# Kernel tuning notes

Hardware: AMD Instinct MI355X
Metric: run time of the kernel (lower is better)

The kernel has to match this reference:

```python
import jax, jax.numpy as jnp
import numpy as np

# ---- static config ----
SCALES = [1, 2, 3, 4, 6, 9, 13, 19, 27, 40, 60, 88, 128]
L = sum(SCALES)            # 400
FIRST_L = SCALES[0]        # 1
C = 1024                   # emb_dim (C == D)
DEPTH = 8
H = 16
DH = C // H
CVAE = 64
V = 4096
ND = 256                   # node_embed_size
MLP = 4 * C
B = 32
EPS = 1e-6

_LVL = np.concatenate([np.full(pn, i, dtype=np.int32) for i, pn in enumerate(SCALES)])  # [L]
_BIAS = np.where(_LVL[:, None] >= _LVL[None, :], 0.0, -np.inf).astype(np.float32)        # [L,L]


def _ln(x):
    # LayerNorm without affine params (VAR's ln_wo_grad), eps=1e-6
    m = jnp.mean(x, axis=-1, keepdims=True)
    v = jnp.mean(jnp.square(x - m), axis=-1, keepdims=True)
    return (x - m) * jax.lax.rsqrt(v + EPS)


def setup_inputs() -> dict:
    key = jax.random.key(0)
    ks = iter(jax.random.split(key, 40))
    def p(shape, s=0.02):
        return jax.random.normal(next(ks), shape, dtype=jnp.float32) * s
    inp = {
        "x_BLCv_wo_first_l": jax.random.normal(next(ks), (B, L - FIRST_L, CVAE), jnp.float32),
        "poc_context": jax.random.normal(next(ks), (B, L, CVAE), jnp.float32),
        "poc_cond": jax.random.normal(next(ks), (B, ND), jnp.float32),
        # embedders / positional
        "word_w": p((CVAE, C)), "word_b": p((C,)),
        "poc_w": p((ND, C)), "poc_b": p((C,)),
        "pos_start": p((1, FIRST_L, C)),
        "pos_1LC": p((1, L, C)),
        "lvl_tab": p((len(SCALES), C)),
        # shared AdaLN (SiLU -> Linear(D, 6C))
        "ada_w": p((C, 6 * C)), "ada_b": p((6 * C,)),
        # per-block params, stacked over depth
        "ada_gss": p((DEPTH, 1, 1, 6, C)),
        "q_w": p((DEPTH, C, C)), "q_b": p((DEPTH, C)),
        "kv_w": p((DEPTH, C, 2 * C)), "kv_b": p((DEPTH, 2 * C)),
        "proj_w": p((DEPTH, C, C)), "proj_b": p((DEPTH, C)),
        "fc1_w": p((DEPTH, C, MLP)), "fc1_b": p((DEPTH, MLP)),
        "fc2_w": p((DEPTH, MLP, C)), "fc2_b": p((DEPTH, C)),
        # AdaLNBeforeHead (SiLU -> Linear(D, 2C)) + head
        "head_ada_w": p((C, 2 * C)), "head_ada_b": p((2 * C,)),
        "head_w": p((C, V)), "head_b": p((V,)),
    }
    return inp


def reference(x_BLCv_wo_first_l, poc_context, poc_cond,
              word_w, word_b, poc_w, poc_b, pos_start, pos_1LC, lvl_tab,
              ada_w, ada_b, ada_gss, q_w, q_b, kv_w, kv_b, proj_w, proj_b,
              fc1_w, fc1_b, fc2_w, fc2_b, head_ada_w, head_ada_b, head_w, head_b):
    lvl_idx = jnp.asarray(_LVL)
    bias = jnp.asarray(_BIAS)                      # [L,L] block scale-causal
    scale = 1.0 / np.sqrt(DH)

    cond = poc_cond @ poc_w + poc_b                # [B,C] (cond_BD == sos source)
    sos = cond[:, None, :] + pos_start             # [B,first_l,C]
    x = jnp.concatenate([sos, x_BLCv_wo_first_l @ word_w + word_b], axis=1)  # [B,L,C]
    lvl = lvl_tab[lvl_idx] + pos_1LC[0]            # [L,C]
    x = x + lvl
    poc = (poc_context @ word_w + word_b) + lvl    # [B,L,C]

    gss = jax.nn.silu(cond) @ ada_w + ada_b        # [B,6C]
    gss = gss.reshape(B, 1, 6, C)

    def block(x, params):
        ag, qw, qb, kvw, kvb, pw, pb, f1w, f1b, f2w, f2b = params
        mod = ag + gss                             # [B,1,6,C]
        g1, g2, s1, s2, sh1, sh2 = [mod[:, :, i] for i in range(6)]  # each [B,1,C]
        # cross-attention (q from modulated x, kv from poc context), scale-causal bias
        xn = _ln(x) * (1.0 + s1) + sh1
        q = (xn @ qw + qb).reshape(B, L, H, DH)
        kv = (poc @ kvw + kvb).reshape(B, L, 2, H, DH)
        k, v = kv[:, :, 0], kv[:, :, 1]
        att = jnp.einsum('bqhd,bkhd->bhqk', q, k) * scale + bias
        att = jax.nn.softmax(att, axis=-1)
        o = jnp.einsum('bhqk,bkhd->bqhd', att, v).reshape(B, L, C)
        x = x + g1 * (o @ pw + pb)
        # FFN with AdaLN modulation
        xn2 = _ln(x) * (1.0 + s2) + sh2
        hdn = jax.nn.gelu(xn2 @ f1w + f1b, approximate=False)
        x = x + g2 * (hdn @ f2w + f2b)
        return x, None

    x, _ = jax.lax.scan(block, x, (ada_gss, q_w, q_b, kv_w, kv_b, proj_w, proj_b,
                                   fc1_w, fc1_b, fc2_w, fc2_b))

    # AdaLNBeforeHead + head
    ss = jax.nn.silu(cond) @ head_ada_w + head_ada_b   # [B,2C]
    h_scale, h_shift = ss[:, None, :C], ss[:, None, C:]
    x = _ln(x) * (1.0 + h_scale) + h_shift
    logits = x @ head_w + head_b                       # [B,L,V]
    return logits
```

## Files before the change

### kernel.cpp

```cpp
#include <hip/hip_runtime.h>
#include <hip/hip_bf16.h>
#include <math.h>

#define DEV __device__ __forceinline__

typedef __attribute__((ext_vector_type(4))) float f32x4;
typedef __attribute__((ext_vector_type(8))) short bf16x8;
typedef __attribute__((ext_vector_type(4))) short s16x4;

static constexpr int Bz = 32, Lz = 400, Cz = 1024, MLPz = 4096;
static constexpr int BL = Bz * Lz;

DEV float bf2f(unsigned short u) {
  union { unsigned int i; float f; } v; v.i = ((unsigned int)u) << 16; return v.f;
}
DEV unsigned short f2bf(float f) {
  union { float f; unsigned int i; } v; v.f = f;
  unsigned int r = v.i + 0x7FFFu + ((v.i >> 16) & 1u);
  return (unsigned short)(r >> 16);
}

DEV int level_of(int l) {
  const int cum[13] = {1,3,6,10,16,25,38,57,84,124,184,272,400};
  int lv = 12;
  #pragma unroll
  for (int i = 12; i >= 0; i--) if (l < cum[i]) lv = i;
  return lv;
}
DEV int row_kmax(int l) {
  const int cum[13] = {1,3,6,10,16,25,38,57,84,124,184,272,400};
  int km = 400;
  #pragma unroll
  for (int i = 12; i >= 0; i--) if (l < cum[i]) km = cum[i];
  return km;
}

DEV void stage16(const unsigned short* g, unsigned short* l) {
#if __has_builtin(__builtin_amdgcn_global_load_lds)
  __builtin_amdgcn_global_load_lds((const __attribute__((address_space(1))) void*)g,
                                   (__attribute__((address_space(3))) void*)l, 16, 0, 0);
#else
  *(bf16x8*)l = *(const bf16x8*)g;
#endif
}

__global__ __launch_bounds__(256)
void tconv_k(const float* __restrict__ in, unsigned short* __restrict__ out, int K, int N)
{
  __shared__ float t[64][65];
  const int n0 = blockIdx.x * 64, k0 = blockIdx.y * 64;
  #pragma unroll
  for (int i = 0; i < 16; i++) {
    int idx = i * 256 + threadIdx.x;
    int r = idx >> 6, c = idx & 63;
    t[r][c] = in[(size_t)(k0 + r) * N + n0 + c];
  }
  __syncthreads();
  #pragma unroll
  for (int i = 0; i < 16; i++) {
    int idx = i * 256 + threadIdx.x;
    int rn = idx >> 6, ck = idx & 63;
    out[(size_t)(n0 + rn) * K + k0 + ck] = f2bf(t[ck][rn]);
  }
}

__global__ __launch_bounds__(256)
void tconv4_k(const float* __restrict__ qw, const float* __restrict__ kvw,
              const float* __restrict__ pjw, const float* __restrict__ f1w,
              unsigned short* __restrict__ qwt, unsigned short* __restrict__ kvwt,
              unsigned short* __restrict__ pjwt, unsigned short* __restrict__ f1wt)
{
  const int z = blockIdx.z;
  const float* in; unsigned short* out; int N;
  if (z == 0)      { in = qw;  out = qwt;  N = 1024; }
  else if (z == 1) { in = kvw; out = kvwt; N = 2048; }
  else if (z == 2) { in = pjw; out = pjwt; N = 1024; }
  else             { in = f1w; out = f1wt; N = 4096; }
  if ((int)blockIdx.x >= (N >> 6)) return;
  __shared__ float t[64][65];
  const int n0 = blockIdx.x * 64, k0 = blockIdx.y * 64;
  #pragma unroll
  for (int i = 0; i < 16; i++) {
    int idx = i * 256 + threadIdx.x;
    int r = idx >> 6, c = idx & 63;
    t[r][c] = in[(size_t)(k0 + r) * N + n0 + c];
  }
  __syncthreads();
  #pragma unroll
  for (int i = 0; i < 16; i++) {
    int idx = i * 256 + threadIdx.x;
    int rn = idx >> 6, ck = idx & 63;
    out[(size_t)(n0 + rn) * 1024 + k0 + ck] = f2bf(t[ck][rn]);
  }
}

enum { EP_BF16 = 0, EP_GELU = 1, EP_RESID = 2, EP_F32 = 3, EP_KV = 4 };

template<int MODE>
__global__ __launch_bounds__(256, 2)
void gemm2_k(const unsigned short* __restrict__ A, const unsigned short* __restrict__ Bt,
             const float* __restrict__ bias, void* __restrict__ out,
             float* __restrict__ xres, const float* __restrict__ gsh,
             const float* __restrict__ gpb, unsigned short* __restrict__ vtb,
             int N, int K)
{
  __shared__ unsigned short As[128 * 64];
  __shared__ unsigned short Bs[128 * 64];
  const int tid = threadIdx.x;
  const int lane = tid & 63, wv = tid >> 6;

  const int nwg = gridDim.x * gridDim.y;
  const int cpx = nwg >> 3;
  const int bid = blockIdx.y * gridDim.x + blockIdx.x;
  const int swz = (bid & 7) * cpx + (bid >> 3);
  const int row0 = (swz % 100) * 128, col0 = (swz / 100) * 128;

  const int wm = (wv >> 1) * 64, wn = (wv & 1) * 64;

  f32x4 acc[4][4] = {};

  for (int k0 = 0; k0 < K; k0 += 64) {
    #pragma unroll
    for (int i = 0; i < 4; i++) {
      int ch = i * 256 + tid;
      int r = ch >> 3;
      int c8 = (ch & 7) ^ (r & 7);
      stage16(A + (size_t)(row0 + r) * K + k0 + c8 * 8, As + ch * 8);
    }
    #pragma unroll
    for (int i = 0; i < 4; i++) {
      int ch = i * 256 + tid;
      int r = ch >> 3;
      int c8 = (ch & 7) ^ (r & 7);
      stage16(Bt + (size_t)(col0 + r) * K + k0 + c8 * 8, Bs + ch * 8);
    }
    __syncthreads();
    #pragma unroll
    for (int kk = 0; kk < 2; kk++) {
      bf16x8 af[4], bfr[4];
      const int bcol = kk * 64 + (lane >> 4) * 16;
      #pragma unroll
      for (int m = 0; m < 4; m++) {
        int r = wm + m * 16 + (lane & 15);
        af[m] = *(const bf16x8*)((char*)As + r * 128 + (bcol ^ ((r & 7) << 4)));
      }
      #pragma unroll
      for (int n = 0; n < 4; n++) {
        int r = wn + n * 16 + (lane & 15);
        bfr[n] = *(const bf16x8*)((char*)Bs + r * 128 + (bcol ^ ((r & 7) << 4)));
      }
      #pragma unroll
      for (int m = 0; m < 4; m++)
        #pragma unroll
        for (int n = 0; n < 4; n++)
          acc[m][n] = __builtin_amdgcn_mfma_f32_16x16x32_bf16(af[m], bfr[n], acc[m][n], 0, 0, 0);
    }
    __syncthreads();
  }

  const int rbase = row0 + wm + ((lane >> 4) << 2);
  const int cbase = col0 + wn + (lane & 15);
  #pragma unroll
  for (int n = 0; n < 4; n++) {
    int gcol = cbase + n * 16;
    float bv = bias[gcol];
    #pragma unroll
    for (int m = 0; m < 4; m++) {
      #pragma unroll
      for (int r = 0; r < 4; r++) {
        int grow = rbase + m * 16 + r;
        float v = acc[m][n][r] + bv;
        if constexpr (MODE == EP_BF16) {
          ((unsigned short*)out)[(size_t)grow * N + gcol] = f2bf(v);
        } else if constexpr (MODE == EP_GELU) {
          float g = 0.5f * v * (1.f + erff(v * 0.70710678118654752f));
          ((unsigned short*)out)[(size_t)grow * N + gcol] = f2bf(g);
        } else if constexpr (MODE == EP_RESID) {
          int b = grow / Lz;
          float g = gsh[gcol] + gpb[(size_t)b * 6144 + gcol];
          xres[(size_t)grow * Cz + gcol] += g * v;
        } else if constexpr (MODE == EP_KV) {
          if (gcol < 1024) {
            ((unsigned short*)out)[(size_t)grow * 1024 + gcol] = f2bf(v);
          } else {
            int b = grow / Lz, l = grow - b * Lz;
            int h = (gcol >> 6) & 15, d = gcol & 63;
            vtb[(((size_t)b * 16 + h) * 64 + d) * Lz + l] = f2bf(v);
          }
        } else {
          ((float*)out)[(size_t)grow * N + gcol] = v;
        }
      }
    }
  }
}

__global__ __launch_bounds__(256)
void ln_k(const float* __restrict__ x, unsigned short* __restrict__ out,
          const float* __restrict__ ssh, const float* __restrict__ spb, int sstride,
          const float* __restrict__ hsh, const float* __restrict__ hpb, int hstride)
{
  const int row = blockIdx.x, tid = threadIdx.x;
  const int b = row / Lz;
  const float* xr = x + (size_t)row * Cz;
  f32x4 v = *(const f32x4*)(xr + tid * 4);
  float s = v[0] + v[1] + v[2] + v[3];
  __shared__ float red[8];
  #pragma unroll
  for (int o = 32; o > 0; o >>= 1) s += __shfl_xor(s, o, 64);
  if ((tid & 63) == 0) red[tid >> 6] = s;
  __syncthreads();
  float mean = (red[0] + red[1] + red[2] + red[3]) * (1.f / 1024.f);
  float vs = 0.f;
  #pragma unroll
  for (int i = 0; i < 4; i++) { float d = v[i] - mean; vs += d * d; }
  #pragma unroll
  for (int o = 32; o > 0; o >>= 1) vs += __shfl_xor(vs, o, 64);
  __syncthreads();
  if ((tid & 63) == 0) red[4 + (tid >> 6)] = vs;
  __syncthreads();
  float var = (red[4] + red[5] + red[6] + red[7]) * (1.f / 1024.f);
  float rstd = rsqrtf(var + 1e-6f);
  #pragma unroll
  for (int i = 0; i < 4; i++) {
    int c = tid * 4 + i;
    float sc = (ssh ? ssh[c] : 0.f) + spb[(size_t)b * sstride + c];
    float sh = (hsh ? hsh[c] : 0.f) + hpb[(size_t)b * hstride + c];
    out[(size_t)row * Cz + c] = f2bf((v[i] - mean) * rstd * (1.f + sc) + sh);
  }
}

__global__ __launch_bounds__(512)
void attn3_k(const unsigned short* __restrict__ qb,
             const unsigned short* __restrict__ kbuf,
             const unsigned short* __restrict__ vtb,
             unsigned short* __restrict__ ob)
{
  __shared__ unsigned short Ks[400 * 64];
  __shared__ unsigned short Vt[64 * 408];
  __shared__ unsigned short Pl[8][512];
  const int bh = blockIdx.x, b = bh >> 4, h = bh & 15;
  const int qc = blockIdx.y;
  const int tid = threadIdx.x;
  const int q0 = qc * 128;
  const int nch = (row_kmax(min(q0 + 127, Lz - 1)) + 15) >> 4;

  const size_t kbase = (size_t)b * Lz * 1024 + h * 64;
  for (int i = tid; i < nch * 128; i += 512) {
    int l = i >> 3, d8 = i & 7;
    bf16x8 kr = *(const bf16x8*)&kbuf[kbase + (size_t)l * 1024 + d8 * 8];
    *(bf16x8*)((char*)Ks + l * 128 + ((d8 * 16) ^ ((l & 7) << 4))) = kr;
  }
  const size_t vbase = ((size_t)b * 16 + h) * 64 * Lz;
  for (int i = tid; i < 64 * 50; i += 512) {
    int d = i / 50, c8 = i - d * 50;
    *(bf16x8*)((char*)Vt + d * 816 + c8 * 16) = *(const bf16x8*)&vtb[vbase + (size_t)d * Lz + c8 * 8];
  }
  __syncthreads();

  const int wv = tid >> 6, lane = tid & 63, g = lane >> 4, q = lane & 15;
  const int qw0 = q0 + wv * 16;
  if (qw0 >= Lz) return;
  const int qrow = qw0 + q;
  const int my_kmax = row_kmax(qrow);
  const int nsch = (row_kmax(qw0 + 15) + 31) >> 5;

  const unsigned short* qp = qb + (size_t)(b * Lz + qrow) * Cz + h * 64;
  bf16x8 qf0 = *(const bf16x8*)(qp + g * 8);
  bf16x8 qf1 = *(const bf16x8*)(qp + 32 + g * 8);
  unsigned short* myP = &Pl[wv][0];

  float m = -1e30f, lsum = 0.f;
  f32x4 acc[4] = {};

  for (int sc = 0; sc < nsch; ++sc) {
    f32x4 st0 = {0.f,0.f,0.f,0.f}, st1 = {0.f,0.f,0.f,0.f};
    {
      int kr = sc * 32 + q;
      const char* kb = (const char*)Ks + kr * 128;
      int sw = (kr & 7) << 4;
      bf16x8 k0 = *(const bf16x8*)(kb + ((g * 16) ^ sw));
      bf16x8 k1 = *(const bf16x8*)(kb + ((64 + g * 16) ^ sw));
      st0 = __builtin_amdgcn_mfma_f32_16x16x32_bf16(k0, qf0, st0, 0, 0, 0);
      st0 = __builtin_amdgcn_mfma_f32_16x16x32_bf16(k1, qf1, st0, 0, 0, 0);
    }
    {
      int kr = sc * 32 + 16 + q;
      const char* kb = (const char*)Ks + kr * 128;
      int sw = (kr & 7) << 4;
      bf16x8 k0 = *(const bf16x8*)(kb + ((g * 16) ^ sw));
      bf16x8 k1 = *(const bf16x8*)(kb + ((64 + g * 16) ^ sw));
      st1 = __builtin_amdgcn_mfma_f32_16x16x32_bf16(k0, qf0, st1, 0, 0, 0);
      st1 = __builtin_amdgcn_mfma_f32_16x16x32_bf16(k1, qf1, st1, 0, 0, 0);
    }

    float s8[8]; float cmax = -1e30f;
    #pragma unroll
    for (int r = 0; r < 4; r++) {
      int k0g = sc * 32 + 4 * g + r;
      int k1g = k0g + 16;
      s8[r]     = (k0g < my_kmax) ? st0[r] * 0.125f : -1e30f;
      s8[4 + r] = (k1g < my_kmax) ? st1[r] * 0.125f : -1e30f;
      cmax = fmaxf(cmax, fmaxf(s8[r], s8[4 + r]));
    }
    cmax = fmaxf(cmax, __shfl_xor(cmax, 16, 64));
    cmax = fmaxf(cmax, __shfl_xor(cmax, 32, 64));
    float mnew = fmaxf(m, cmax);
    float f = __expf(m - mnew);
    float p[8], ps = 0.f;
    #pragma unroll
    for (int r = 0; r < 8; r++) { p[r] = __expf(s8[r] - mnew); ps += p[r]; }
    ps += __shfl_xor(ps, 16, 64);
    ps += __shfl_xor(ps, 32, 64);
    lsum = lsum * f + ps;
    m = mnew;
    #pragma unroll
    for (int blk = 0; blk < 4; blk++)
      #pragma unroll
      for (int j = 0; j < 4; j++) acc[blk][j] *= f;

    #pragma unroll
    for (int cp = 0; cp < 2; cp++) {
      #pragma unroll
      for (int j = 0; j < 2; j++) {
        unsigned int lo = f2bf(p[4 * cp + 2 * j]);
        unsigned int hi = f2bf(p[4 * cp + 2 * j + 1]);
        int w = 8 * cp + 2 * g + j;
        *(unsigned int*)((char*)myP + q * 64 + 4 * (w ^ q)) = lo | (hi << 16);
      }
    }

    unsigned int pw[4];
    #pragma unroll
    for (int i = 0; i < 4; i++)
      pw[i] = *(const unsigned int*)((const char*)myP + q * 64 + 4 * ((4 * g + i) ^ q));
    bf16x8 pfrag;
    #pragma unroll
    for (int i = 0; i < 4; i++) {
      pfrag[2 * i]     = (short)(pw[i] & 0xFFFF);
      pfrag[2 * i + 1] = (short)(pw[i] >> 16);
    }

    #pragma unroll
    for (int blk = 0; blk < 4; blk++) {
      bf16x8 vf = *(const bf16x8*)((const char*)Vt + (16 * blk + q) * 816 + (sc * 32 + 8 * g) * 2);
      acc[blk] = __builtin_amdgcn_mfma_f32_16x16x32_bf16(vf, pfrag, acc[blk], 0, 0, 0);
    }
  }

  float inv = 1.f / lsum;
  unsigned short* op = ob + (size_t)(b * Lz + qrow) * Cz + h * 64;
  #pragma unroll
  for (int blk = 0; blk < 4; blk++)
    #pragma unroll
    for (int r = 0; r < 4; r++)
      op[16 * blk + 4 * g + r] = f2bf(acc[blk][r] * inv);
}

__global__ __launch_bounds__(256)
void cond_k(const float* __restrict__ pc, const float* __restrict__ pw,
            const float* __restrict__ pb, float* __restrict__ cond,
            float* __restrict__ silu)
{
  const int b = blockIdx.y;
  const int n = blockIdx.x * 256 + threadIdx.x;
  __shared__ float a[256];
  a[threadIdx.x] = pc[b * 256 + threadIdx.x];
  __syncthreads();
  float s = pb[n];
  for (int k = 0; k < 256; k++) s += a[k] * pw[(size_t)k * Cz + n];
  cond[(size_t)b * Cz + n] = s;
  silu[(size_t)b * Cz + n] = s / (1.f + __expf(-s));
}

__global__ __launch_bounds__(256)
void smallmm_k(const float* __restrict__ A, const float* __restrict__ W,
               const float* __restrict__ bias, float* __restrict__ out, int N)
{
  const int b = blockIdx.y;
  const int n = blockIdx.x * 256 + threadIdx.x;
  __shared__ float a[1024];
  for (int i = threadIdx.x; i < 1024; i += 256) a[i] = A[(size_t)b * 1024 + i];
  __syncthreads();
  float s = bias[n];
  for (int k = 0; k < 1024; k++) s += a[k] * W[(size_t)k * N + n];
  out[(size_t)b * N + n] = s;
}

template<int MODE>
__global__ __launch_bounds__(256)
void embed_k(const float* __restrict__ src, const float* __restrict__ ww,
             const float* __restrict__ wb, const float* __restrict__ cond,
             const float* __restrict__ pos_start, const float* __restrict__ pos1,
             const float* __restrict__ ltab, void* __restrict__ out)
{
  const int r0 = blockIdx.x * 4;
  const int tid = threadIdx.x;
  const int b = r0 / Lz;
  __shared__ float a[4][64];
  {
    int rr = tid >> 6, k = tid & 63;
    int l = (r0 + rr) % Lz;
    float val;
    if (MODE == 0) val = (l == 0) ? 0.f : src[((size_t)b * (Lz - 1) + (l - 1)) * 64 + k];
    else           val = src[((size_t)(r0 + rr)) * 64 + k];
    a[rr][k] = val;
  }
  __syncthreads();
  #pragma unroll
  for (int ci = 0; ci < 4; ci++) {
    int c = tid + ci * 256;
    float s[4];
    #pragma unroll
    for (int rr = 0; rr < 4; rr++) {
      int l = (r0 + rr) % Lz;
      s[rr] = wb[c] + ltab[(size_t)level_of(l) * Cz + c] + pos1[(size_t)l * Cz + c];
    }
    for (int k = 0; k < 64; k++) {
      float w = ww[(size_t)k * Cz + c];
      #pragma unroll
      for (int rr = 0; rr < 4; rr++) s[rr] += a[rr][k] * w;
    }
    #pragma unroll
    for (int rr = 0; rr < 4; rr++) {
      int l = (r0 + rr) % Lz;
      if (MODE == 0) {
        float val = s[rr];
        if (l == 0) val = cond[(size_t)b * Cz + c] + pos_start[c] + ltab[c] + pos1[c];
        ((float*)out)[((size_t)(r0 + rr)) * Cz + c] = val;
      } else {
        ((unsigned short*)out)[((size_t)(r0 + rr)) * Cz + c] = f2bf(s[rr]);
      }
    }
  }
}

extern "C" void kernel_launch(void* const* d_in, const int* in_sizes, int n_in,
                              void* d_out, int out_size, void* d_ws, size_t ws_size,
                              hipStream_t stream)
{
  (void)in_sizes; (void)n_in; (void)out_size; (void)ws_size;
  const float* x_blcv   = (const float*)d_in[0];
  const float* poc_ctx  = (const float*)d_in[1];
  const float* poc_cond = (const float*)d_in[2];
  const float* word_w   = (const float*)d_in[3];
  const float* word_b   = (const float*)d_in[4];
  const float* poc_w    = (const float*)d_in[5];
  const float* poc_b    = (const float*)d_in[6];
  const float* pos_start= (const float*)d_in[7];
  const float* pos_1lc  = (const float*)d_in[8];
  const float* lvl_tab  = (const float*)d_in[9];
  const float* ada_w    = (const float*)d_in[10];
  const float* ada_b    = (const float*)d_in[11];
  const float* ada_gss  = (const float*)d_in[12];
  const float* q_w      = (const float*)d_in[13];
  const float* q_b      = (const float*)d_in[14];
  const float* kv_w     = (const float*)d_in[15];
  const float* kv_b     = (const float*)d_in[16];
  const float* proj_w   = (const float*)d_in[17];
  const float* proj_b   = (const float*)d_in[18];
  const float* fc1_w    = (const float*)d_in[19];
  const float* fc1_b    = (const float*)d_in[20];
  const float* fc2_w    = (const float*)d_in[21];
  const float* fc2_b    = (const float*)d_in[22];
  const float* head_ada_w = (const float*)d_in[23];
  const float* head_ada_b = (const float*)d_in[24];
  const float* head_w   = (const float*)d_in[25];
  const float* head_b   = (const float*)d_in[26];

  char* p = (char*)d_ws;
  auto carve = [&](size_t bytes) { void* r = (void*)p; p += (bytes + 255) & ~(size_t)255; return r; };
  float* x            = (float*)carve((size_t)BL * Cz * 4);
  unsigned short* xn  = (unsigned short*)carve((size_t)BL * Cz * 2);
  unsigned short* poc = (unsigned short*)carve((size_t)BL * Cz * 2);
  unsigned short* qbf = (unsigned short*)carve((size_t)BL * Cz * 2);
  unsigned short* kbuf= (unsigned short*)carve((size_t)BL * Cz * 2);
  unsigned short* vtb = (unsigned short*)carve((size_t)BL * Cz * 2);
  unsigned short* ob  = (unsigned short*)carve((size_t)BL * Cz * 2);
  unsigned short* hdn = (unsigned short*)carve((size_t)BL * MLPz * 2);
  unsigned short* wt  = (unsigned short*)carve((size_t)12582912 * 2);
  float* cond  = (float*)carve(32 * 1024 * 4);
  float* siluc = (float*)carve(32 * 1024 * 4);
  float* gss   = (float*)carve(32 * 6144 * 4);
  float* ss    = (float*)carve(32 * 2048 * 4);

  unsigned short* qwt  = wt;
  unsigned short* kvwt = wt + 1048576;
  unsigned short* pjwt = wt + 3145728;
  unsigned short* f1wt = wt + 4194304;
  unsigned short* f2wt = wt + 8388608;

  cond_k<<<dim3(4, 32), 256, 0, stream>>>(poc_cond, poc_w, poc_b, cond, siluc);
  smallmm_k<<<dim3(24, 32), 256, 0, stream>>>(siluc, ada_w, ada_b, gss, 6144);
  smallmm_k<<<dim3(8, 32), 256, 0, stream>>>(siluc, head_ada_w, head_ada_b, ss, 2048);
  embed_k<0><<<3200, 256, 0, stream>>>(x_blcv, word_w, word_b, cond, pos_start, pos_1lc, lvl_tab, x);
  embed_k<1><<<3200, 256, 0, stream>>>(poc_ctx, word_w, word_b, cond, pos_start, pos_1lc, lvl_tab, poc);

  for (int d = 0; d < 8; d++) {
    const float* ag = ada_gss + (size_t)d * 6144;
    tconv4_k<<<dim3(64, 16, 4), 256, 0, stream>>>(
        q_w + (size_t)d * 1048576, kv_w + (size_t)d * 2097152,
        proj_w + (size_t)d * 1048576, fc1_w + (size_t)d * 4194304,
        qwt, kvwt, pjwt, f1wt);
    tconv_k<<<dim3(16, 64), 256, 0, stream>>>(fc2_w + (size_t)d * 4194304, f2wt, 4096, 1024);

    ln_k<<<BL, 256, 0, stream>>>(x, xn, ag + 2 * 1024, gss + 2 * 1024, 6144,
                                 ag + 4 * 1024, gss + 4 * 1024, 6144);
    gemm2_k<EP_BF16><<<dim3(100, 8), 256, 0, stream>>>(
        xn, qwt, q_b + d * 1024, qbf, nullptr, nullptr, nullptr, nullptr, 1024, 1024);
    gemm2_k<EP_KV><<<dim3(100, 16), 256, 0, stream>>>(
        poc, kvwt, kv_b + d * 2048, kbuf, nullptr, nullptr, nullptr, vtb, 2048, 1024);
    attn3_k<<<dim3(512, 4), 512, 0, stream>>>(qbf, kbuf, vtb, ob);
    gemm2_k<EP_RESID><<<dim3(100, 8), 256, 0, stream>>>(
        ob, pjwt, proj_b + d * 1024, nullptr, x, ag + 0, gss + 0, nullptr, 1024, 1024);
    ln_k<<<BL, 256, 0, stream>>>(x, xn, ag + 3 * 1024, gss + 3 * 1024, 6144,
                                 ag + 5 * 1024, gss + 5 * 1024, 6144);
    gemm2_k<EP_GELU><<<dim3(100, 32), 256, 0, stream>>>(
        xn, f1wt, fc1_b + d * 4096, hdn, nullptr, nullptr, nullptr, nullptr, 4096, 1024);
    gemm2_k<EP_RESID><<<dim3(100, 8), 256, 0, stream>>>(
        hdn, f2wt, fc2_b + d * 1024, nullptr, x, ag + 1024, gss + 1024, nullptr, 1024, 4096);
  }
  ln_k<<<BL, 256, 0, stream>>>(x, xn, nullptr, ss, 2048, nullptr, ss + 1024, 2048);
  tconv_k<<<dim3(64, 16), 256, 0, stream>>>(head_w, wt, 1024, 4096);
  gemm2_k<EP_F32><<<dim3(100, 32), 256, 0, stream>>>(
      xn, wt, head_b, d_out, nullptr, nullptr, nullptr, nullptr, 4096, 1024);
}
```

Before: 6.781 ms.

## Drop GEMM tile swizzle, vectorize LN store, trim attention V staging and rescaling

The GEMM replaces its XCD-aware block swizzle with plain blockIdx row/column mapping. The LayerNorm-modulate kernel now packs four bf16 outputs into one vector store. The attention kernel stages only the V columns the query chunk needs, clamps V fragment offsets to that range, and skips the online-softmax rescale when the running max does not grow by more than a threshold. It also converts P to bf16 with a packed hardware instruction. The lazy rescale and the smaller -30000 mask constant risk numeric differences, and removing the swizzle may hurt L2 locality across chiplets.

```diff
diff --git a/kernel.cpp b/kernel.cpp
--- a/kernel.cpp
+++ b/kernel.cpp
@@ -108,13 +108,7 @@
   __shared__ unsigned short Bs[128 * 64];
   const int tid = threadIdx.x;
   const int lane = tid & 63, wv = tid >> 6;
-
-  const int nwg = gridDim.x * gridDim.y;
-  const int cpx = nwg >> 3;
-  const int bid = blockIdx.y * gridDim.x + blockIdx.x;
-  const int swz = (bid & 7) * cpx + (bid >> 3);
-  const int row0 = (swz % 100) * 128, col0 = (swz / 100) * 128;
-
+  const int row0 = blockIdx.x * 128, col0 = blockIdx.y * 128;
   const int wm = (wv >> 1) * 64, wn = (wv & 1) * 64;
 
   f32x4 acc[4][4] = {};
@@ -221,13 +215,15 @@
   __syncthreads();
   float var = (red[4] + red[5] + red[6] + red[7]) * (1.f / 1024.f);
   float rstd = rsqrtf(var + 1e-6f);
+  s16x4 o4;
   #pragma unroll
   for (int i = 0; i < 4; i++) {
     int c = tid * 4 + i;
     float sc = (ssh ? ssh[c] : 0.f) + spb[(size_t)b * sstride + c];
     float sh = (hsh ? hsh[c] : 0.f) + hpb[(size_t)b * hstride + c];
-    out[(size_t)row * Cz + c] = f2bf((v[i] - mean) * rstd * (1.f + sc) + sh);
-  }
+    o4[i] = (short)f2bf((v[i] - mean) * rstd * (1.f + sc) + sh);
+  }
+  *(s16x4*)(&out[(size_t)row * Cz + tid * 4]) = o4;
 }
 
 __global__ __launch_bounds__(512)
@@ -252,8 +248,9 @@
     *(bf16x8*)((char*)Ks + l * 128 + ((d8 * 16) ^ ((l & 7) << 4))) = kr;
   }
   const size_t vbase = ((size_t)b * 16 + h) * 64 * Lz;
-  for (int i = tid; i < 64 * 50; i += 512) {
-    int d = i / 50, c8 = i - d * 50;
+  const int vch = nch * 2;
+  for (int i = tid; i < 64 * vch; i += 512) {
+    int d = i / vch, c8 = i - d * vch;
     *(bf16x8*)((char*)Vt + d * 816 + c8 * 16) = *(const bf16x8*)&vtb[vbase + (size_t)d * Lz + c8 * 8];
   }
   __syncthreads();
@@ -264,13 +261,14 @@
   const int qrow = qw0 + q;
   const int my_kmax = row_kmax(qrow);
   const int nsch = (row_kmax(qw0 + 15) + 31) >> 5;
+  const int vclamp = nch * 16 - 8;
 
   const unsigned short* qp = qb + (size_t)(b * Lz + qrow) * Cz + h * 64;
   bf16x8 qf0 = *(const bf16x8*)(qp + g * 8);
   bf16x8 qf1 = *(const bf16x8*)(qp + 32 + g * 8);
   unsigned short* myP = &Pl[wv][0];
 
-  float m = -1e30f, lsum = 0.f;
+  float m = -30000.f, lsum = 0.f;
   f32x4 acc[4] = {};
 
   for (int sc = 0; sc < nsch; ++sc) {
@@ -294,39 +292,45 @@
       st1 = __builtin_amdgcn_mfma_f32_16x16x32_bf16(k1, qf1, st1, 0, 0, 0);
     }
 
-    float s8[8]; float cmax = -1e30f;
+    float s8[8]; float cmax = -30000.f;
     #pragma unroll
     for (int r = 0; r < 4; r++) {
       int k0g = sc * 32 + 4 * g + r;
       int k1g = k0g + 16;
-      s8[r]     = (k0g < my_kmax) ? st0[r] * 0.125f : -1e30f;
-      s8[4 + r] = (k1g < my_kmax) ? st1[r] * 0.125f : -1e30f;
+      s8[r]     = (k0g < my_kmax) ? st0[r] * 0.125f : -30000.f;
+      s8[4 + r] = (k1g < my_kmax) ? st1[r] * 0.125f : -30000.f;
       cmax = fmaxf(cmax, fmaxf(s8[r], s8[4 + r]));
     }
     cmax = fmaxf(cmax, __shfl_xor(cmax, 16, 64));
     cmax = fmaxf(cmax, __shfl_xor(cmax, 32, 64));
-    float mnew = fmaxf(m, cmax);
-    float f = __expf(m - mnew);
+
+    if (!__all(cmax <= m + 8.f)) {
+      float mnew = fmaxf(m, cmax);
+      float f = __expf(m - mnew);
+      lsum *= f;
+      #pragma unroll
+      for (int blk = 0; blk < 4; blk++)
+        #pragma unroll
+        for (int j = 0; j < 4; j++) acc[blk][j] *= f;
+      m = mnew;
+    }
+
     float p[8], ps = 0.f;
     #pragma unroll
-    for (int r = 0; r < 8; r++) { p[r] = __expf(s8[r] - mnew); ps += p[r]; }
+    for (int r = 0; r < 8; r++) { p[r] = __expf(s8[r] - m); ps += p[r]; }
     ps += __shfl_xor(ps, 16, 64);
     ps += __shfl_xor(ps, 32, 64);
-    lsum = lsum * f + ps;
-    m = mnew;
-    #pragma unroll
-    for (int blk = 0; blk < 4; blk++)
-      #pragma unroll
-      for (int j = 0; j < 4; j++) acc[blk][j] *= f;
+    lsum += ps;
 
     #pragma unroll
     for (int cp = 0; cp < 2; cp++) {
       #pragma unroll
       for (int j = 0; j < 2; j++) {
-        unsigned int lo = f2bf(p[4 * cp + 2 * j]);
-        unsigned int hi = f2bf(p[4 * cp + 2 * j + 1]);
+        unsigned int pk;
+        asm("v_cvt_pk_bf16_f32 %0, %1, %2" : "=v"(pk)
+            : "v"(p[4 * cp + 2 * j]), "v"(p[4 * cp + 2 * j + 1]));
         int w = 8 * cp + 2 * g + j;
-        *(unsigned int*)((char*)myP + q * 64 + 4 * (w ^ q)) = lo | (hi << 16);
+        *(unsigned int*)((char*)myP + q * 64 + 4 * (w ^ q)) = pk;
       }
     }
 
@@ -341,9 +345,10 @@
       pfrag[2 * i + 1] = (short)(pw[i] >> 16);
     }
 
+    const int koff = min(sc * 32 + 8 * g, vclamp);
     #pragma unroll
     for (int blk = 0; blk < 4; blk++) {
-      bf16x8 vf = *(const bf16x8*)((const char*)Vt + (16 * blk + q) * 816 + (sc * 32 + 8 * g) * 2);
+      bf16x8 vf = *(const bf16x8*)((const char*)Vt + (16 * blk + q) * 816 + koff * 2);
       acc[blk] = __builtin_amdgcn_mfma_f32_16x16x32_bf16(vf, pfrag, acc[blk], 0, 0, 0);
     }
   }
```

After: 6.410 ms. 5.5% less time.
